# Optimization experiments

Hardware: AMD Instinct MI355X
Metric: run time of the kernel (lower is better)

Reference implementation:

```python
import jax, jax.numpy as jnp
import numpy as np

N_NODES = 10000
N_EDGES = 320000
N_REL = 460
N_BASES = 30
D = 200


def setup_inputs() -> dict:
    key = jax.random.key(0)
    k = jax.random.split(key, 8)
    x = jax.random.normal(k[0], (N_NODES, D), dtype=jnp.float32)
    edge_index = jax.random.randint(k[1], (2, N_EDGES), 0, N_NODES, dtype=jnp.int32)
    edge_type = jax.random.randint(k[2], (N_EDGES,), 0, N_REL, dtype=jnp.int32)
    # Xavier-uniform-like init scales
    w_bound = float(np.sqrt(6.0 / (D + D)))
    c_bound = float(np.sqrt(6.0 / (N_REL + N_BASES)))
    weight = jax.random.uniform(k[3], (N_BASES, D, D), minval=-w_bound, maxval=w_bound, dtype=jnp.float32)
    coeff = jax.random.uniform(k[4], (N_REL, N_BASES), minval=-c_bound, maxval=c_bound, dtype=jnp.float32)
    self_weight = jax.random.uniform(k[5], (D, D), minval=-w_bound, maxval=w_bound, dtype=jnp.float32)
    bias = jnp.zeros((D,), dtype=jnp.float32)
    return {
        "x": x,
        "weight": weight,
        "coeff": coeff,
        "self_weight": self_weight,
        "bias": bias,
        "edge_index": edge_index,
        "edge_type": edge_type,
        "num_nodes": N_NODES,
    }


def reference(x, weight, coeff, self_weight, bias, edge_index, edge_type, num_nodes):
    # RelationalGraphConv.forward:
    #   W_r = sum_b coeff[r, b] * V_b ; msg_e = x[src_e] @ W_{type_e}
    #   out[n] = (sum_{e: tgt_e = n} msg_e) / max(in_deg[n], 1) + x @ W_self + bias
    src = edge_index[0]
    tgt = edge_index[1]
    src_feats = x[src]                    # (E, d_in) gather
    edge_coeff = coeff[edge_type]         # (E, B) gather

    # msg_e = sum_b coeff[type_e, b] * (src_e @ V_b): scan over bases to avoid
    # materializing an (E, B, d_out) intermediate (same math as W_r = coeff @ V).
    def body(acc, inputs):
        Vb, cb = inputs                   # (d_in, d_out), (E,)
        return acc + (src_feats @ Vb) * cb[:, None], None

    msg0 = jnp.zeros((src.shape[0], weight.shape[2]), dtype=x.dtype)
    msg, _ = jax.lax.scan(body, msg0, (weight, edge_coeff.T))  # (E, d_out)

    out = jax.ops.segment_sum(msg, tgt, num_segments=num_nodes)              # (N, d_out)
    deg = jax.ops.segment_sum(jnp.ones_like(tgt, dtype=x.dtype), tgt, num_segments=num_nodes)
    out = out / jnp.clip(deg, 1.0)[:, None]
    out = out + x @ self_weight + bias
    return out
```

## Files before the change

kernel.cpp:

```cpp
#include <hip/hip_runtime.h>
#include <hip/hip_bf16.h>

#define N_NODES 10000
#define N_EDGES 320000
#define N_REL   460
#define N_BASES 30
#define DIM     200
#define KZ      6016
#define KT      6240
#define NSTEPS  195
#define NTILES  157
#define NFRAG   16
#define KSPLIT  8
#define PROWS   10048
#define TKELEM  2048

#define PREP_B8 (NFRAG * NSTEPS * 64)
#define PREP_C  (N_REL * 16)
#define PREP_X8 (N_NODES * 28)
#define S1_TOTAL (N_EDGES + PREP_B8 + PREP_C)
#define S2_TOTAL (N_EDGES + PREP_X8)

using short8  = __attribute__((ext_vector_type(8))) short;
using s4v     = __attribute__((ext_vector_type(4))) short;
using floatx4 = __attribute__((ext_vector_type(4))) float;

__device__ __forceinline__ unsigned short f2bf(float f) {
    union { float f; unsigned u; } v; v.f = f;
    unsigned u = v.u;
    return (unsigned short)((u + 0x7fffu + ((u >> 16) & 1u)) >> 16);
}

__device__ __forceinline__ float bf2f(unsigned short s) {
    union { unsigned u; float f; } v;
    v.u = ((unsigned)s) << 16;
    return v.f;
}

__device__ __forceinline__ short8 pack8(const unsigned short* u) {
    union { unsigned short s[8]; short8 v; } p;
#pragma unroll
    for (int i = 0; i < 8; ++i) p.s[i] = u[i];
    return p.v;
}

__device__ __forceinline__ size_t asw_idx(int n, int c) {
    int t = n >> 6, sub = (n >> 4) & 3, rl = n & 15;
    int kk = c >> 5, w = c & 31;
    return (size_t)(t * NSTEPS + kk) * TKELEM + sub * 512 + rl * 32 + w;
}


__global__ void sort1_kernel(const int* __restrict__ tgt, int* __restrict__ deg,
                             const float* __restrict__ weight, const float* __restrict__ sw,
                             const float* __restrict__ coeff,
                             unsigned short* __restrict__ BSW, unsigned int* __restrict__ Cpair) {
    int idx = blockIdx.x * blockDim.x + threadIdx.x;
    if (idx < N_EDGES) {
        atomicAdd(&deg[tgt[idx]], 1);
        return;
    }
    idx -= N_EDGES;
    if (idx < PREP_B8) {
        int f = idx / (NSTEPS * 64);
        int rem = idx - f * (NSTEPS * 64);
        int kk = rem >> 6;
        int l = rem & 63;
        int rB = f * 16 + (l & 15);
        int kbase = kk * 32 + (l >> 4) * 8;
        unsigned short bs[8];
#pragma unroll
        for (int j = 0; j < 8; ++j) {
            int k = kbase + j;
            float v = 0.f;
            if (rB < DIM) {
                if (k < KZ) {
                    if (k < N_BASES * DIM) {
                        int b = k / DIM, kc = k - b * DIM;
                        v = weight[(b * DIM + kc) * DIM + rB];
                    }
                } else {
                    int jj = k - KZ;
                    if (jj < DIM) v = sw[jj * DIM + rB];
                }
            }
            bs[j] = f2bf(v);
        }
        *(short8*)(BSW + (size_t)idx * 8) = pack8(bs);
        return;
    }
    idx -= PREP_B8;
    if (idx < PREP_C) {
        int t = idx >> 4, m = idx & 15;
        unsigned lo = f2bf(coeff[t * N_BASES + m]);
        unsigned hi = (m + 16 < N_BASES) ? f2bf(coeff[t * N_BASES + m + 16]) : 0u;
        Cpair[idx] = lo | (hi << 16);
    }
}

__global__ __launch_bounds__(1024) void scan_kernel(const int* deg, int* starts,
                                                    int* cursor, float* dinv) {
    __shared__ int part[1024];
    int tid = threadIdx.x;
    const int PER = (N_NODES + 1023) / 1024;
    int base = tid * PER;
    int s = 0;
    for (int i = 0; i < PER; ++i) { int idx = base + i; if (idx < N_NODES) s += deg[idx]; }
    part[tid] = s; __syncthreads();
    for (int off = 1; off < 1024; off <<= 1) {
        int v = (tid >= off) ? part[tid - off] : 0;
        __syncthreads();
        part[tid] += v;
        __syncthreads();
    }
    int run = (tid > 0) ? part[tid - 1] : 0;
    for (int i = 0; i < PER; ++i) {
        int idx = base + i;
        if (idx < N_NODES) {
            int d = deg[idx];
            starts[idx] = run; cursor[idx] = run;
            dinv[idx] = 1.0f / (float)(d > 0 ? d : 1);
            run += d;
        }
    }
    if (tid == 1023) starts[N_NODES] = part[1023];
}


__global__ void sort2_kernel(const int* __restrict__ src, const int* __restrict__ tgt,
                             const int* __restrict__ etype, int* __restrict__ cursor,
                             int2* __restrict__ sedge,
                             const float* __restrict__ x, const int* __restrict__ deg,
                             unsigned short* __restrict__ XbfP, unsigned short* __restrict__ ASW) {
    int idx = blockIdx.x * blockDim.x + threadIdx.x;
    if (idx < N_EDGES) {
        int t = tgt[idx];
        int pos = atomicAdd(&cursor[t], 1);
        sedge[pos] = make_int2(src[idx], etype[idx]);
        return;
    }
    idx -= N_EDGES;
    if (idx < PREP_X8) {
        int n = idx / 28, t = idx - n * 28;
        int p = t >> 2, c4 = (t & 3) << 2;
        int cl = p * 32 + c4;
        int ch = cl + 16;
        int d = deg[n]; if (d < 1) d = 1;
        float df = (float)d;
        floatx4 vlo = (floatx4){0.f, 0.f, 0.f, 0.f};
        floatx4 vhi = (floatx4){0.f, 0.f, 0.f, 0.f};
        if (cl < DIM) vlo = *(const floatx4*)(x + (size_t)n * DIM + cl);
        if (ch < DIM) vhi = *(const floatx4*)(x + (size_t)n * DIM + ch);
        unsigned short xp[8], asl[4], ash[4];
#pragma unroll
        for (int i = 0; i < 4; ++i) {
            xp[2 * i]     = f2bf(vlo[i]);
            xp[2 * i + 1] = f2bf(vhi[i]);
            asl[i] = f2bf(df * vlo[i]);
            ash[i] = f2bf(df * vhi[i]);
        }
        *(short8*)(XbfP + (size_t)n * 224 + p * 32 + c4 * 2) = pack8(xp);
        union { unsigned short s[4]; s4v v; } ul, uh;
#pragma unroll
        for (int i = 0; i < 4; ++i) { ul.s[i] = asl[i]; uh.s[i] = ash[i]; }
        *(s4v*)(ASW + asw_idx(n, KZ + cl)) = ul.v;
        *(s4v*)(ASW + asw_idx(n, KZ + ch)) = uh.v;
    }
}


__global__ __launch_bounds__(256) void agg_kernel(const unsigned int* __restrict__ XbfP,
                                                  const unsigned int* __restrict__ Cpair,
                                                  const int* __restrict__ starts,
                                                  const int2* __restrict__ sedge,
                                                  unsigned short* __restrict__ ASW) {
    __shared__ __align__(16) unsigned short zbuf[4][3232];
    int lane = threadIdx.x & 63;
    int wave = threadIdx.x >> 6;
    int n = blockIdx.x * 4 + wave;
    int ln = lane & 15, q = lane >> 4;

    floatx4 acc0[13], acc1[13];
#pragma unroll
    for (int f = 0; f < 13; ++f) {
        acc0[f] = (floatx4){0.f, 0.f, 0.f, 0.f};
        acc1[f] = acc0[f];
    }

    int e0 = starts[n], e1 = starts[n + 1];
    for (int kb = e0; kb < e1; kb += 32) {
        int eb = kb + 8 * q;
        unsigned short a0v[8], a1v[8];
        int srcs[8];
#pragma unroll
        for (int j = 0; j < 8; ++j) {
            int e = eb + j;
            int ec = (e < e1) ? e : (e1 - 1);
            int2 sd = sedge[ec];
            unsigned cp = (e < e1) ? Cpair[sd.y * 16 + ln] : 0u;
            a0v[j] = (unsigned short)(cp & 0xffffu);
            a1v[j] = (unsigned short)(cp >> 16);
            srcs[j] = sd.x;
        }
        short8 A0 = pack8(a0v), A1 = pack8(a1v);

        unsigned pv[2][8];
#pragma unroll
        for (int j = 0; j < 8; ++j)
            pv[0][j] = XbfP[(size_t)srcs[j] * 112 + ln];
#pragma unroll
        for (int p = 0; p < 7; ++p) {
            int cur = p & 1, nxt = cur ^ 1;
            if (p < 6) {
#pragma unroll
                for (int j = 0; j < 8; ++j)
                    pv[nxt][j] = XbfP[(size_t)srcs[j] * 112 + (p + 1) * 16 + ln];
            }
            unsigned short lo[8], hi[8];
#pragma unroll
            for (int j = 0; j < 8; ++j) {
                lo[j] = (unsigned short)(pv[cur][j] & 0xffffu);
                hi[j] = (unsigned short)(pv[cur][j] >> 16);
            }
            short8 Blo = pack8(lo), Bhi = pack8(hi);
            int f0 = 2 * p;
            acc0[f0] = __builtin_amdgcn_mfma_f32_16x16x32_bf16(A0, Blo, acc0[f0], 0, 0, 0);
            acc1[f0] = __builtin_amdgcn_mfma_f32_16x16x32_bf16(A1, Blo, acc1[f0], 0, 0, 0);
            if (2 * p + 1 < 13) {
                acc0[2 * p + 1] = __builtin_amdgcn_mfma_f32_16x16x32_bf16(A0, Bhi, acc0[2 * p + 1], 0, 0, 0);
                acc1[2 * p + 1] = __builtin_amdgcn_mfma_f32_16x16x32_bf16(A1, Bhi, acc1[2 * p + 1], 0, 0, 0);
            }
        }
    }

    unsigned short* zb = zbuf[wave];
    int t = n >> 6, sub = (n >> 4) & 3, rl = n & 15;
    const uint4* zb4 = (const uint4*)zb;
    uint4* dst = (uint4*)ASW;
    size_t base_u4 = (size_t)t * NSTEPS * 256 + sub * 64 + rl * 4;

#pragma unroll
    for (int f = 0; f < 13; ++f) {
        int d = f * 16 + ln;
        if (d < DIM) {
#pragma unroll
            for (int i = 0; i < 4; ++i)
                zb[(q * 4 + i) * DIM + d] = f2bf(acc0[f][i]);
        }
    }
    for (int v = lane; v < 400; v += 64) {
        int kk = v >> 2, w8 = v & 3;
        dst[base_u4 + (size_t)kk * 256 + w8] = zb4[v];
    }

    if (lane < 16) zb[2800 + lane] = 0;
#pragma unroll
    for (int f = 0; f < 13; ++f) {
        int d = f * 16 + ln;
        if (d < DIM) {
#pragma unroll
            for (int i = 0; i < 4; ++i) {
                int b1 = 16 + q * 4 + i;
                if (b1 < N_BASES) zb[(b1 - 16) * DIM + d] = f2bf(acc1[f][i]);
            }
        }
    }
    for (int v = lane; v < 352; v += 64) {
        int kk = 100 + (v >> 2), w8 = v & 3;
        dst[base_u4 + (size_t)kk * 256 + w8] = zb4[v];
    }
}


#define GITER(VLIT, BU, BL, KK)                                                        \
  {                                                                                    \
    asm volatile("s_waitcnt vmcnt(" #VLIT ")" ::: "memory");                           \
    __builtin_amdgcn_sched_barrier(0);                                                 \
    asm volatile("s_barrier" ::: "memory");                                            \
    const int kk_ = (KK);                                                              \
    const int kld_ = (kk_ + 1 < ke) ? kk_ + 1 : ke - 1;                                \
    BL[0] = *(const short8*)(pb + ((size_t)(0 * 4 * NSTEPS) + kld_) * 512);            \
    BL[1] = *(const short8*)(pb + ((size_t)(1 * 4 * NSTEPS) + kld_) * 512);            \
    BL[2] = *(const short8*)(pb + ((size_t)(2 * 4 * NSTEPS) + kld_) * 512);            \
    BL[3] = *(const short8*)(pb + ((size_t)(3 * 4 * NSTEPS) + kld_) * 512);            \
    const int kst_ = (kk_ + 3 < ke) ? kk_ + 3 : ke - 1;                                \
    __builtin_amdgcn_global_load_lds(                                                  \
        (const unsigned int*)(aswt + (size_t)kst_ * TKELEM + goff),                    \
        (unsigned int*)(ldsw + ((kk_ + 3) & 3) * 2048), 16, 0, 0);                     \
    const unsigned short* sp_ = alds + (kk_ & 3) * 2048 + pread8;                      \
    short8 av0 = *(const short8*)(sp_);                                                \
    short8 av1 = *(const short8*)(sp_ + 512);                                          \
    short8 av2 = *(const short8*)(sp_ + 1024);                                         \
    short8 av3 = *(const short8*)(sp_ + 1536);                                         \
    _Pragma("unroll")                                                                  \
    for (int i_ = 0; i_ < 4; ++i_) {                                                   \
      acc[i_][0] = __builtin_amdgcn_mfma_f32_16x16x32_bf16(av0, BU[i_], acc[i_][0], 0, 0, 0); \
      acc[i_][1] = __builtin_amdgcn_mfma_f32_16x16x32_bf16(av1, BU[i_], acc[i_][1], 0, 0, 0); \
      acc[i_][2] = __builtin_amdgcn_mfma_f32_16x16x32_bf16(av2, BU[i_], acc[i_][2], 0, 0, 0); \
      acc[i_][3] = __builtin_amdgcn_mfma_f32_16x16x32_bf16(av3, BU[i_], acc[i_][3], 0, 0, 0); \
    }                                                                                  \
  }

__global__ __launch_bounds__(256, 4) void gemm_kernel(const unsigned short* __restrict__ ASW,
                                                      const unsigned short* __restrict__ BSW,
                                                      unsigned short* __restrict__ part) {
    __shared__ __align__(16) unsigned short alds[4 * 2048];
    int tid = threadIdx.x;
    int lane = tid & 63, wave = tid >> 6;
    int tile = blockIdx.x, chunk = blockIdx.y;
    int ks = (chunk * NSTEPS) / KSPLIT;
    int ke = ((chunk + 1) * NSTEPS) / KSPLIT;
    int ln = lane & 15, q = lane >> 4;

    const unsigned short* aswt = ASW + (size_t)tile * NSTEPS * TKELEM;
    const unsigned short* pb = BSW + (size_t)(wave * NSTEPS) * 512 + lane * 8;

    int gsw = (tid & 0xE0) | ((tid & 7) << 2) | ((tid >> 3) & 3);
    int goff = gsw * 8;
    int pread8 = ((((ln >> 3) & 1) << 5) | (q << 3) | (ln & 7)) * 8;
    unsigned short* ldsw = alds + wave * 512;

    floatx4 acc[4][4];
#pragma unroll
    for (int i = 0; i < 4; ++i)
#pragma unroll
        for (int s = 0; s < 4; ++s) acc[i][s] = (floatx4){0.f, 0.f, 0.f, 0.f};

    short8 bA[4], bB[4];

#pragma unroll
    for (int i = 0; i < 4; ++i)
        bA[i] = *(const short8*)(pb + ((size_t)(i * 4 * NSTEPS) + ks) * 512);
#pragma unroll
    for (int d = 0; d < 3; ++d)
        __builtin_amdgcn_global_load_lds(
            (const unsigned int*)(aswt + (size_t)(ks + d) * TKELEM + goff),
            (unsigned int*)(ldsw + ((ks + d) & 3) * 2048), 16, 0, 0);

    GITER(0, bA, bB, ks + 0);
    GITER(4, bB, bA, ks + 1);
    GITER(8, bA, bB, ks + 2);

    int kk = ks + 3;
    for (; kk + 1 < ke; kk += 2) {
        GITER(8, bB, bA, kk);
        GITER(8, bA, bB, kk + 1);
    }
    if (kk < ke) { GITER(8, bB, bA, kk); }

    int row0 = tile * 64;
    unsigned short* pbase = part + ((size_t)chunk * PROWS + row0) * 208;
#pragma unroll
    for (int i = 0; i < 4; ++i) {
        int fg = wave + 4 * i;
        if (fg < 13) {
            int c = fg * 16 + ln;
#pragma unroll
            for (int s = 0; s < 4; ++s)
#pragma unroll
                for (int ii = 0; ii < 4; ++ii)
                    pbase[(s * 16 + q * 4 + ii) * 208 + c] = f2bf(acc[i][s][ii]);
        }
    }
}


__global__ __launch_bounds__(256) void reduce_kernel(const unsigned short* __restrict__ part,
                                                     const float* __restrict__ dinv,
                                                     const float* __restrict__ bias,
                                                     float* __restrict__ out) {
    int idx = blockIdx.x * blockDim.x + threadIdx.x;
    if (idx >= N_NODES * 50) return;
    int r = idx / 50, cq = idx - r * 50;
    float s0 = 0.f, s1 = 0.f, s2 = 0.f, s3 = 0.f;
#pragma unroll
    for (int c = 0; c < KSPLIT; ++c) {
        union { unsigned short s[4]; s4v v; } u;
        u.v = *(const s4v*)(part + ((size_t)c * PROWS + r) * 208 + cq * 4);
        s0 += bf2f(u.s[0]); s1 += bf2f(u.s[1]);
        s2 += bf2f(u.s[2]); s3 += bf2f(u.s[3]);
    }
    float dv = dinv[r];
    float4 b = *(const float4*)(bias + cq * 4);
    float4 o;
    o.x = s0 * dv + b.x; o.y = s1 * dv + b.y;
    o.z = s2 * dv + b.z; o.w = s3 * dv + b.w;
    *(float4*)(out + (size_t)r * DIM + cq * 4) = o;
}


extern "C" void kernel_launch(void* const* d_in, const int* in_sizes, int n_in,
                              void* d_out, int out_size, void* d_ws, size_t ws_size,
                              hipStream_t stream) {
    const float* x      = (const float*)d_in[0];
    const float* weight = (const float*)d_in[1];
    const float* coeff  = (const float*)d_in[2];
    const float* selfw  = (const float*)d_in[3];
    const float* bias   = (const float*)d_in[4];
    const int*   eidx   = (const int*)d_in[5];
    const int*   etype  = (const int*)d_in[6];
    const int* src = eidx;
    const int* tgt = eidx + N_EDGES;
    float* out = (float*)d_out;

    char* ws = (char*)d_ws;
    size_t off = 0;
    auto carve = [&](size_t bytes) {
        char* p = ws + off;
        off += (bytes + 255) & ~(size_t)255;
        return p;
    };
    unsigned short* ASW  = (unsigned short*)carve((size_t)NTILES * NSTEPS * TKELEM * 2);
    unsigned short* BSW  = (unsigned short*)carve((size_t)NFRAG * NSTEPS * 512 * 2);
    unsigned short* part = (unsigned short*)carve((size_t)KSPLIT * PROWS * 208 * 2);
    unsigned short* XbfP = (unsigned short*)carve((size_t)(N_NODES * 224 + 64) * 2);
    unsigned int*  Cpair = (unsigned int*)carve((size_t)N_REL * 16 * 4);
    int*   deg    = (int*)carve((size_t)N_NODES * 4);
    int*   starts = (int*)carve((size_t)(N_NODES + 1) * 4);
    int*   cursor = (int*)carve((size_t)N_NODES * 4);
    float* dinv   = (float*)carve((size_t)N_NODES * 4);
    int2*  sedge  = (int2*)carve((size_t)N_EDGES * 8);

    hipMemsetAsync(deg, 0, (size_t)N_NODES * 4, stream);

    sort1_kernel<<<(S1_TOTAL + 255) / 256, 256, 0, stream>>>(
        tgt, deg, weight, selfw, coeff, BSW, Cpair);

    scan_kernel<<<1, 1024, 0, stream>>>(deg, starts, cursor, dinv);

    sort2_kernel<<<(S2_TOTAL + 255) / 256, 256, 0, stream>>>(
        src, tgt, etype, cursor, sedge, x, deg, XbfP, ASW);

    agg_kernel<<<N_NODES / 4, 256, 0, stream>>>(
        (const unsigned int*)XbfP, Cpair, starts, sedge, ASW);

    dim3 ggrid(NTILES, KSPLIT);
    gemm_kernel<<<ggrid, 256, 0, stream>>>(ASW, BSW, part);

    reduce_kernel<<<(N_NODES * 50 + 255) / 256, 256, 0, stream>>>(part, dinv, bias, out);
}
```

Before: 247.8 us.

## Split agg_kernel per-node work across two waves by basis half

Each node is now handled by two waves rather than one, and each wave computes only one half of the basis-coefficient outputs (bases 0-15 or 16-29). This halves the accumulator registers per wave and doubles the grid size, aiming for higher occupancy and more parallelism on the edge aggregation. The cost is that both waves gather the same source features and edge data, so gather traffic and index loads are duplicated.

```diff
diff --git a/kernel.cpp b/kernel.cpp
--- a/kernel.cpp
+++ b/kernel.cpp
@@ -177,20 +177,18 @@
     __shared__ __align__(16) unsigned short zbuf[4][3232];
     int lane = threadIdx.x & 63;
     int wave = threadIdx.x >> 6;
-    int n = blockIdx.x * 4 + wave;
+    int n = blockIdx.x * 2 + (wave >> 1);
+    int h = wave & 1;
     int ln = lane & 15, q = lane >> 4;
 
-    floatx4 acc0[13], acc1[13];
-#pragma unroll
-    for (int f = 0; f < 13; ++f) {
-        acc0[f] = (floatx4){0.f, 0.f, 0.f, 0.f};
-        acc1[f] = acc0[f];
-    }
+    floatx4 acc[13];
+#pragma unroll
+    for (int f = 0; f < 13; ++f) acc[f] = (floatx4){0.f, 0.f, 0.f, 0.f};
 
     int e0 = starts[n], e1 = starts[n + 1];
     for (int kb = e0; kb < e1; kb += 32) {
         int eb = kb + 8 * q;
-        unsigned short a0v[8], a1v[8];
+        unsigned short av[8];
         int srcs[8];
 #pragma unroll
         for (int j = 0; j < 8; ++j) {
@@ -198,11 +196,10 @@
             int ec = (e < e1) ? e : (e1 - 1);
             int2 sd = sedge[ec];
             unsigned cp = (e < e1) ? Cpair[sd.y * 16 + ln] : 0u;
-            a0v[j] = (unsigned short)(cp & 0xffffu);
-            a1v[j] = (unsigned short)(cp >> 16);
+            av[j] = h ? (unsigned short)(cp >> 16) : (unsigned short)(cp & 0xffffu);
             srcs[j] = sd.x;
         }
-        short8 A0 = pack8(a0v), A1 = pack8(a1v);
+        short8 A = pack8(av);
 
         unsigned pv[2][8];
 #pragma unroll
@@ -224,12 +221,9 @@
             }
             short8 Blo = pack8(lo), Bhi = pack8(hi);
             int f0 = 2 * p;
-            acc0[f0] = __builtin_amdgcn_mfma_f32_16x16x32_bf16(A0, Blo, acc0[f0], 0, 0, 0);
-            acc1[f0] = __builtin_amdgcn_mfma_f32_16x16x32_bf16(A1, Blo, acc1[f0], 0, 0, 0);
-            if (2 * p + 1 < 13) {
-                acc0[2 * p + 1] = __builtin_amdgcn_mfma_f32_16x16x32_bf16(A0, Bhi, acc0[2 * p + 1], 0, 0, 0);
-                acc1[2 * p + 1] = __builtin_amdgcn_mfma_f32_16x16x32_bf16(A1, Bhi, acc1[2 * p + 1], 0, 0, 0);
-            }
+            acc[f0] = __builtin_amdgcn_mfma_f32_16x16x32_bf16(A, Blo, acc[f0], 0, 0, 0);
+            if (2 * p + 1 < 13)
+                acc[2 * p + 1] = __builtin_amdgcn_mfma_f32_16x16x32_bf16(A, Bhi, acc[2 * p + 1], 0, 0, 0);
         }
     }
 
@@ -239,35 +233,37 @@
     uint4* dst = (uint4*)ASW;
     size_t base_u4 = (size_t)t * NSTEPS * 256 + sub * 64 + rl * 4;
 
-#pragma unroll
-    for (int f = 0; f < 13; ++f) {
-        int d = f * 16 + ln;
-        if (d < DIM) {
-#pragma unroll
-            for (int i = 0; i < 4; ++i)
-                zb[(q * 4 + i) * DIM + d] = f2bf(acc0[f][i]);
-        }
-    }
-    for (int v = lane; v < 400; v += 64) {
-        int kk = v >> 2, w8 = v & 3;
-        dst[base_u4 + (size_t)kk * 256 + w8] = zb4[v];
-    }
-
-    if (lane < 16) zb[2800 + lane] = 0;
-#pragma unroll
-    for (int f = 0; f < 13; ++f) {
-        int d = f * 16 + ln;
-        if (d < DIM) {
-#pragma unroll
-            for (int i = 0; i < 4; ++i) {
-                int b1 = 16 + q * 4 + i;
-                if (b1 < N_BASES) zb[(b1 - 16) * DIM + d] = f2bf(acc1[f][i]);
+    if (h == 0) {
+#pragma unroll
+        for (int f = 0; f < 13; ++f) {
+            int d = f * 16 + ln;
+            if (d < DIM) {
+#pragma unroll
+                for (int i = 0; i < 4; ++i)
+                    zb[(q * 4 + i) * DIM + d] = f2bf(acc[f][i]);
             }
         }
-    }
-    for (int v = lane; v < 352; v += 64) {
-        int kk = 100 + (v >> 2), w8 = v & 3;
-        dst[base_u4 + (size_t)kk * 256 + w8] = zb4[v];
+        for (int v = lane; v < 400; v += 64) {
+            int kk = v >> 2, w8 = v & 3;
+            dst[base_u4 + (size_t)kk * 256 + w8] = zb4[v];
+        }
+    } else {
+        if (lane < 16) zb[2800 + lane] = 0;
+#pragma unroll
+        for (int f = 0; f < 13; ++f) {
+            int d = f * 16 + ln;
+            if (d < DIM) {
+#pragma unroll
+                for (int i = 0; i < 4; ++i) {
+                    int b1 = 16 + q * 4 + i;
+                    if (b1 < N_BASES) zb[(q * 4 + i) * DIM + d] = f2bf(acc[f][i]);
+                }
+            }
+        }
+        for (int v = lane; v < 352; v += 64) {
+            int kk = 100 + (v >> 2), w8 = v & 3;
+            dst[base_u4 + (size_t)kk * 256 + w8] = zb4[v];
+        }
     }
 }
 
@@ -431,7 +427,7 @@
     sort2_kernel<<<(S2_TOTAL + 255) / 256, 256, 0, stream>>>(
         src, tgt, etype, cursor, sedge, x, deg, XbfP, ASW);
 
-    agg_kernel<<<N_NODES / 4, 256, 0, stream>>>(
+    agg_kernel<<<N_NODES / 2, 256, 0, stream>>>(
         (const unsigned int*)XbfP, Cpair, starts, sedge, ASW);
 
     dim3 ggrid(NTILES, KSPLIT);
```

New measurement: 241.3 us (median of 2 runs). 1.03x faster.
